# Optimization experiments

Hardware: AMD Instinct MI355X
Metric: run time of the kernel (lower is better)

The kernel has to match this reference:

```python
import jax, jax.numpy as jnp
import numpy as np

B, CIN, COUT, H, W = 32, 64, 64, 58, 58
RSIZE, NB, EDIM = 512, 10, 64


def setup_inputs() -> dict:
    key = jax.random.key(0)
    ks = jax.random.split(key, 8)
    return {
        "x": jax.random.normal(ks[0], (B, CIN, H, W), jnp.float32),
        "routing_vector": jax.random.normal(ks[1], (B, RSIZE), jnp.float32),
        "W1": jax.random.normal(ks[2], (RSIZE, 128), jnp.float32) * 0.02,
        "b1": jnp.zeros((128,), jnp.float32),
        "W2": jax.random.normal(ks[3], (128, EDIM), jnp.float32) * 0.05,
        "b2": jnp.zeros((EDIM,), jnp.float32),
        "emb": jax.random.normal(ks[4], (NB, EDIM), jnp.float32),
        "conv_w": jax.random.normal(ks[5], (NB, COUT, CIN, 3, 3), jnp.float32) * 0.02,
        "conv_b": jnp.zeros((NB, COUT), jnp.float32),
    }


def _cosine_similarity(a, b):
    # calculate_similarity assumed cosine: [B,E] x [N,E] -> [B,N]
    a = a / (jnp.linalg.norm(a, axis=-1, keepdims=True) + 1e-8)
    b = b / (jnp.linalg.norm(b, axis=-1, keepdims=True) + 1e-8)
    return a @ b.T


def reference(x, routing_vector, W1, b1, W2, b2, emb, conv_w, conv_b):
    # process_routing: Linear(512,128) -> ReLU -> Linear(128,64)
    r = jax.nn.relu(routing_vector @ W1 + b1) @ W2 + b2          # [B, 64]
    sim = _cosine_similarity(r, emb)                              # [B, NB]
    # eval mode: no noise; SIMPLESampler treated as identity on softmax weights
    weights = jax.nn.softmax(sim, axis=-1)                        # [B, NB]
    # run all NB expert convs as one valid 3x3 conv with NB*COUT output channels
    w_all = conv_w.reshape(NB * COUT, CIN, 3, 3)
    y = jax.lax.conv_general_dilated(
        x, w_all, window_strides=(1, 1), padding='VALID',
        dimension_numbers=('NCHW', 'OIHW', 'NCHW'))               # [B, NB*COUT, 56, 56]
    y = y + conv_b.reshape(1, NB * COUT, 1, 1)
    y = y.reshape(B, NB, COUT, y.shape[-2], y.shape[-1])          # [B, NB, COUT, 56, 56]
    # weighted mixture over experts; softmax weights sum to 1 (d in torch code)
    d = jnp.sum(weights, axis=-1)                                 # [B]
    out = jnp.einsum('bnchw,bn->bchw', y, weights) / d[:, None, None, None]
    return out
```

## Files before the change

kernel.cpp:

```cpp
#include <hip/hip_runtime.h>
#include <hip/hip_bf16.h>
#include <stdint.h>

#define BATCH 32
#define CIN   64
#define COUT  64
#define HIN   58
#define WIN   58
#define HOUT  56
#define WOUT  56
#define RSIZE 512
#define NB    10
#define EDIM  64
#define HID   128
#define CHW   (HIN*WIN)
#define OHW   (HOUT*WOUT)

typedef __attribute__((ext_vector_type(8)))  short short8;
typedef __attribute__((ext_vector_type(16))) float f32x16;

__device__ __forceinline__ unsigned short f2bf(float f) {
    unsigned int u = __builtin_bit_cast(unsigned int, f);
    u += 0x7fffu + ((u >> 16) & 1u);
    return (unsigned short)(u >> 16);
}

__global__ __launch_bounds__(512) void route_kernel(
    const float* __restrict__ rv, const float* __restrict__ W1,
    const float* __restrict__ b1, const float* __restrict__ W2,
    const float* __restrict__ b2, const float* __restrict__ emb,
    float* __restrict__ wts)
{
    const int b = blockIdx.x;
    const int t = threadIdx.x;

    __shared__ float s_rv[RSIZE];
    __shared__ float s_part[4 * HID];
    __shared__ float s_h[HID];
    __shared__ float s_r[EDIM];
    __shared__ float s_rn;
    __shared__ float s_sim[NB];

    if (t < 128) ((float4*)s_rv)[t] = ((const float4*)(rv + (size_t)b * RSIZE))[t];
    __syncthreads();

    {
        const int h = t & 127, kq = t >> 7;
        float acc = 0.0f;
        const float* wp = W1 + (size_t)(kq * 128) * HID + h;
        const float* xp = s_rv + kq * 128;
        #pragma unroll 8
        for (int k = 0; k < 128; ++k) acc = fmaf(xp[k], wp[(size_t)k * HID], acc);
        s_part[kq * HID + h] = acc;
    }
    __syncthreads();
    if (t < HID)
        s_h[t] = fmaxf(s_part[t] + s_part[HID + t] + s_part[2 * HID + t] +
                       s_part[3 * HID + t] + b1[t], 0.0f);
    __syncthreads();

    {
        const int e = t & 63, kq = t >> 6;
        float acc = 0.0f;
        const float* wp = W2 + (size_t)(kq * 16) * EDIM + e;
        const float* hp = s_h + kq * 16;
        #pragma unroll
        for (int k = 0; k < 16; ++k) acc = fmaf(hp[k], wp[(size_t)k * EDIM], acc);
        s_part[kq * 64 + e] = acc;
    }
    __syncthreads();
    if (t < EDIM) {
        float r = b2[t];
        #pragma unroll
        for (int q = 0; q < 8; ++q) r += s_part[q * 64 + t];
        s_r[t] = r;
    }
    __syncthreads();

    if (t < 64) {
        float sq = s_r[t] * s_r[t];
        #pragma unroll
        for (int off = 32; off; off >>= 1) sq += __shfl_xor(sq, off);
        if (t == 0) s_rn = sqrtf(sq);
    }
    __syncthreads();

    {
        const int wid = t >> 6, lane = t & 63;
        for (int n = wid; n < NB; n += 8) {
            const float ev = emb[n * EDIM + lane];
            float dot = ev * s_r[lane];
            float nb2 = ev * ev;
            #pragma unroll
            for (int off = 32; off; off >>= 1) {
                dot += __shfl_xor(dot, off);
                nb2 += __shfl_xor(nb2, off);
            }
            if (lane == 0)
                s_sim[n] = dot / ((s_rn + 1e-8f) * (sqrtf(nb2) + 1e-8f));
        }
    }
    __syncthreads();

    if (t == 0) {
        float m = -1e30f;
        #pragma unroll
        for (int n = 0; n < NB; ++n) m = fmaxf(m, s_sim[n]);
        float w[NB], sum = 0.0f;
        #pragma unroll
        for (int n = 0; n < NB; ++n) { w[n] = __expf(s_sim[n] - m); sum += w[n]; }
        const float inv = 1.0f / sum;
        float d = 0.0f;
        #pragma unroll
        for (int n = 0; n < NB; ++n) { w[n] *= inv; d += w[n]; }
        const float invd = 1.0f / d;
        #pragma unroll
        for (int n = 0; n < NB; ++n) wts[b * NB + n] = w[n] * invd;
    }
}

__global__ __launch_bounds__(256) void wmix2_kernel(
    const float* __restrict__ cw, const float* __restrict__ cbias,
    const float* __restrict__ wts,
    unsigned short* __restrict__ weffb, float* __restrict__ sbias_g)
{
    const int co = blockIdx.x & 63;
    const int bq = blockIdx.x >> 6;
    const int t  = threadIdx.x;

    __shared__ float scw[NB * 576];
    __shared__ float s_w[8 * NB];

    if (t < 8 * NB) s_w[t] = wts[bq * 8 * NB + t];
    for (int i = t; i < 1440; i += 256) {
        const int n = i / 144, r4 = i - n * 144;
        ((float4*)scw)[(size_t)n * 144 + r4] =
            *(const float4*)(cw + (size_t)(n * COUT + co) * 576 + r4 * 4);
    }
    __syncthreads();

    for (int i = t; i < 8 * 576; i += 256) {
        const int bl  = i / 576, rem = i - bl * 576;
        const int s   = rem >> 6, cin = rem & 63;
        float v = 0.0f;
        #pragma unroll
        for (int n = 0; n < NB; ++n)
            v = fmaf(s_w[bl * NB + n], scw[n * 576 + cin * 9 + s], v);
        const int b  = bq * 8 + bl;
        const int ks = cin >> 4, kg = (cin >> 3) & 1, c8 = cin & 7;
        weffb[((((size_t)(b * 9 + s) * 4 + ks) * 2 + kg) * 64 + co) * 8 + c8] = f2bf(v);
    }
    if (t < 8) {
        float v = 0.0f;
        #pragma unroll
        for (int n = 0; n < NB; ++n) v = fmaf(s_w[t * NB + n], cbias[n * COUT + co], v);
        sbias_g[(bq * 8 + t) * COUT + co] = v;
    }
}

__global__ __launch_bounds__(256, 2) void conv3_kernel(
    const float* __restrict__ x, const unsigned short* __restrict__ weffb,
    const float* __restrict__ sbias_g, float* __restrict__ out)
{
    const int bid  = blockIdx.x;
    const int xcd  = bid & 7;
    const int slot = bid >> 3;
    const int b    = xcd + 8 * (slot / 28);
    const int tile = slot - (slot / 28) * 28;
    const int oh0  = tile * 2;

    const int t    = threadIdx.x;
    const int wid  = t >> 6;
    const int lane = t & 63;
    const int ln   = lane & 31;
    const int kg   = lane >> 5;

    __shared__ unsigned short xs[232 * 64];
    __shared__ float sbias[COUT];

    if (t < COUT) sbias[t] = sbias_g[b * COUT + t];

    const float* xg = x + (size_t)b * CIN * CHW + oh0 * WIN;
    #pragma unroll
    for (int k = 0; k < 8; ++k) {
        const int e = t + 256 * k;
        if (e < 1856) {
            const int cb = e / 232;
            const int sp = e - cb * 232;
            const float* gp = xg + (size_t)(cb * 8) * CHW + sp;
            short8 v;
            #pragma unroll
            for (int j = 0; j < 8; ++j)
                v[j] = (short)f2bf(gp[(size_t)j * CHW]);
            *(short8*)&xs[sp * 64 + (cb ^ (sp & 7)) * 8] = v;
        }
    }
    __syncthreads();

    const int p   = wid * 32 + ln;
    const bool valid = (p < 112);
    const int pc  = valid ? p : 111;
    const int r   = pc / 56, ow = pc - r * 56;
    const int sbase = r * WIN + ow;

    f32x16 acc[2];
    #pragma unroll
    for (int mt = 0; mt < 2; ++mt)
        #pragma unroll
        for (int j = 0; j < 16; ++j) acc[mt][j] = 0.0f;

    #pragma unroll
    for (int ks = 0; ks < 4; ++ks) {
        #pragma unroll
        for (int s = 0; s < 9; ++s) {
            const int kh = s / 3, kw = s - kh * 3;
            const unsigned short* ap =
                weffb + (((size_t)(b * 9 + s) * 4 + ks) * 2 + kg) * 512;
            const short8 a0 = *(const short8*)(ap + ln * 8);
            const short8 a1 = *(const short8*)(ap + (32 + ln) * 8);
            const int sp   = sbase + kh * WIN + kw;
            const int addr = (sp << 7) + ((((ks << 1) + kg) ^ (sp & 7)) << 4);
            const short8 bf = *(const short8*)((const char*)xs + addr);
            acc[0] = __builtin_amdgcn_mfma_f32_32x32x16_bf16(a0, bf, acc[0], 0, 0, 0);
            acc[1] = __builtin_amdgcn_mfma_f32_32x32x16_bf16(a1, bf, acc[1], 0, 0, 0);
        }
    }

    if (valid) {
        #pragma unroll
        for (int mt = 0; mt < 2; ++mt) {
            float* op = out + ((size_t)(b * COUT + mt * 32) * HOUT + oh0 + r) * WOUT + ow;
            #pragma unroll
            for (int reg = 0; reg < 16; ++reg) {
                const int co_l = (reg & 3) + 8 * (reg >> 2) + 4 * kg;
                op[(size_t)co_l * OHW] = acc[mt][reg] + sbias[mt * 32 + co_l];
            }
        }
    }
}

extern "C" void kernel_launch(void* const* d_in, const int* in_sizes, int n_in,
                              void* d_out, int out_size, void* d_ws, size_t ws_size,
                              hipStream_t stream) {
    const float* x    = (const float*)d_in[0];
    const float* rv   = (const float*)d_in[1];
    const float* W1   = (const float*)d_in[2];
    const float* b1   = (const float*)d_in[3];
    const float* W2   = (const float*)d_in[4];
    const float* b2   = (const float*)d_in[5];
    const float* emb  = (const float*)d_in[6];
    const float* cw   = (const float*)d_in[7];
    const float* cb   = (const float*)d_in[8];
    float* out = (float*)d_out;

    float* wts            = (float*)d_ws;
    float* sbias_g        = (float*)d_ws + 1024;
    unsigned short* weffb = (unsigned short*)((float*)d_ws + 3072);

    route_kernel<<<dim3(BATCH), dim3(512), 0, stream>>>(rv, W1, b1, W2, b2, emb, wts);
    wmix2_kernel<<<dim3(256), dim3(256), 0, stream>>>(cw, cb, wts, weffb, sbias_g);
    conv3_kernel<<<dim3(BATCH * 28), dim3(256), 0, stream>>>(x, weffb, sbias_g, out);
}
```

Baseline: 40.65 us.

## Split conv waves by output-channel half and batch A-fragment loads per K-slice

Reassigns the four waves of the conv kernel so each handles one 32-channel output half over two 32-pixel tiles, instead of both channel halves over one pixel tile. Weight fragments for all 9 taps of a K-slice are loaded up front into registers, halving per-wave global weight loads. This costs twice as many LDS reads of the input fragments and more live registers, and wasted work on out-of-range pixel tiles remains.

```diff
diff --git a/kernel.cpp b/kernel.cpp
--- a/kernel.cpp
+++ b/kernel.cpp
@@ -158,7 +158,7 @@
     }
 }
 
-__global__ __launch_bounds__(256, 2) void conv3_kernel(
+__global__ __launch_bounds__(256, 2) void conv4_kernel(
     const float* __restrict__ x, const unsigned short* __restrict__ weffb,
     const float* __restrict__ sbias_g, float* __restrict__ out)
 {
@@ -174,6 +174,8 @@
     const int lane = t & 63;
     const int ln   = lane & 31;
     const int kg   = lane >> 5;
+    const int mt   = wid & 1;
+    const int nh   = wid >> 1;
 
     __shared__ unsigned short xs[232 * 64];
     __shared__ float sbias[COUT];
@@ -197,44 +199,57 @@
     }
     __syncthreads();
 
-    const int p   = wid * 32 + ln;
-    const bool valid = (p < 112);
-    const int pc  = valid ? p : 111;
-    const int r   = pc / 56, ow = pc - r * 56;
-    const int sbase = r * WIN + ow;
+    int sbase[2]; int pq[2]; bool val[2];
+    #pragma unroll
+    for (int nt = 0; nt < 2; ++nt) {
+        const int p = (nh * 2 + nt) * 32 + ln;
+        val[nt] = (p < 112);
+        const int pc = val[nt] ? p : 111;
+        pq[nt] = pc;
+        const int r = pc / 56, ow = pc - r * 56;
+        sbase[nt] = r * WIN + ow;
+    }
 
     f32x16 acc[2];
     #pragma unroll
-    for (int mt = 0; mt < 2; ++mt)
-        #pragma unroll
-        for (int j = 0; j < 16; ++j) acc[mt][j] = 0.0f;
+    for (int nt = 0; nt < 2; ++nt)
+        #pragma unroll
+        for (int j = 0; j < 16; ++j) acc[nt][j] = 0.0f;
+
+    const unsigned short* abase =
+        weffb + (size_t)b * 36864 + kg * 512 + (mt * 32 + ln) * 8;
 
     #pragma unroll
     for (int ks = 0; ks < 4; ++ks) {
+        short8 af[9];
+        #pragma unroll
+        for (int s = 0; s < 9; ++s)
+            af[s] = *(const short8*)(abase + (size_t)s * 4096 + ks * 1024);
+
         #pragma unroll
         for (int s = 0; s < 9; ++s) {
             const int kh = s / 3, kw = s - kh * 3;
-            const unsigned short* ap =
-                weffb + (((size_t)(b * 9 + s) * 4 + ks) * 2 + kg) * 512;
-            const short8 a0 = *(const short8*)(ap + ln * 8);
-            const short8 a1 = *(const short8*)(ap + (32 + ln) * 8);
-            const int sp   = sbase + kh * WIN + kw;
-            const int addr = (sp << 7) + ((((ks << 1) + kg) ^ (sp & 7)) << 4);
-            const short8 bf = *(const short8*)((const char*)xs + addr);
-            acc[0] = __builtin_amdgcn_mfma_f32_32x32x16_bf16(a0, bf, acc[0], 0, 0, 0);
-            acc[1] = __builtin_amdgcn_mfma_f32_32x32x16_bf16(a1, bf, acc[1], 0, 0, 0);
-        }
-    }
-
-    if (valid) {
-        #pragma unroll
-        for (int mt = 0; mt < 2; ++mt) {
-            float* op = out + ((size_t)(b * COUT + mt * 32) * HOUT + oh0 + r) * WOUT + ow;
+            const int off = kh * WIN + kw;
             #pragma unroll
-            for (int reg = 0; reg < 16; ++reg) {
-                const int co_l = (reg & 3) + 8 * (reg >> 2) + 4 * kg;
-                op[(size_t)co_l * OHW] = acc[mt][reg] + sbias[mt * 32 + co_l];
+            for (int nt = 0; nt < 2; ++nt) {
+                const int sp   = sbase[nt] + off;
+                const int addr = (sp << 7) + ((((ks << 1) + kg) ^ (sp & 7)) << 4);
+                const short8 bf = *(const short8*)((const char*)xs + addr);
+                acc[nt] = __builtin_amdgcn_mfma_f32_32x32x16_bf16(af[s], bf, acc[nt], 0, 0, 0);
             }
+        }
+    }
+
+    #pragma unroll
+    for (int nt = 0; nt < 2; ++nt) {
+        if (!val[nt]) continue;
+        const int p = pq[nt];
+        const int r = p / 56, ow = p - r * 56;
+        float* op = out + ((size_t)(b * COUT + mt * 32) * HOUT + oh0 + r) * WOUT + ow;
+        #pragma unroll
+        for (int reg = 0; reg < 16; ++reg) {
+            const int co_l = (reg & 3) + 8 * (reg >> 2) + 4 * kg;
+            op[(size_t)co_l * OHW] = acc[nt][reg] + sbias[mt * 32 + co_l];
         }
     }
 }
@@ -259,5 +274,5 @@
 
     route_kernel<<<dim3(BATCH), dim3(512), 0, stream>>>(rv, W1, b1, W2, b2, emb, wts);
     wmix2_kernel<<<dim3(256), dim3(256), 0, stream>>>(cw, cb, wts, weffb, sbias_g);
-    conv3_kernel<<<dim3(BATCH * 28), dim3(256), 0, stream>>>(x, weffb, sbias_g, out);
-}
+    conv4_kernel<<<dim3(BATCH * 28), dim3(256), 0, stream>>>(x, weffb, sbias_g, out);
+}
```

After: 39.54 us. 1.03x faster.
